# Kernel optimization log

Hardware: AMD Instinct MI355X
Metric: run time of the kernel (lower is better)

The kernel has to match this reference:

```python
import jax, jax.numpy as jnp
import numpy as np

N, R, IN_DIM, OUT_DIM, MODE = 16, 128, 64, 64, 16


def setup_inputs() -> dict:
    key = jax.random.key(0)
    k1, k2, k3, k4, k5 = jax.random.split(key, 5)
    # xavier_normal-like scale used by the torch init:
    # std = gain * sqrt(2/(fan_in+fan_out)) with gain = sqrt(in+out)/(in*out)
    fan = IN_DIM * OUT_DIM * MODE * MODE  # torch fans over last-dim slices; scale is tiny either way
    w_std = (1.0 / (IN_DIM * OUT_DIM)) * np.sqrt(IN_DIM + OUT_DIM)
    return {
        "X": jax.random.normal(k1, (N, R, R, IN_DIM), dtype=jnp.float32),
        "w_res": jax.random.normal(k2, (IN_DIM, OUT_DIM), dtype=jnp.float32) / np.sqrt(IN_DIM),
        "b_res": jax.random.normal(k3, (OUT_DIM,), dtype=jnp.float32) * 0.01,
        "fw0": jax.random.normal(k4, (IN_DIM, OUT_DIM, MODE, MODE, 2), dtype=jnp.float32) * w_std,
        "fw1": jax.random.normal(k5, (IN_DIM, OUT_DIM, MODE, MODE, 2), dtype=jnp.float32) * w_std,
    }


def reference(X, w_res, b_res, fw0, fw1):
    # X: [N, r, r, in_dim]
    n, r, _, _ = X.shape
    m = MODE
    res = X @ w_res + b_res                          # [N, r, r, out]
    Xp = jnp.transpose(X, (0, 3, 1, 2))              # [N, in, r, r]
    X_ft = jnp.fft.rfft2(Xp, s=(r, r), norm="ortho")  # [N, in, r, r//2+1] complex
    W0 = fw0[..., 0] + 1j * fw0[..., 1]              # [in, out, m, m] complex
    W1 = fw1[..., 0] + 1j * fw1[..., 1]
    top = jnp.einsum("nihw,iohw->nohw", X_ft[:, :, :m, :m], W0)
    bot = jnp.einsum("nihw,iohw->nohw", X_ft[:, :, -m:, :m], W1)
    Out_ft = jnp.zeros((n, OUT_DIM, r, r // 2 + 1), dtype=top.dtype)
    Out_ft = Out_ft.at[:, :, :m, :m].set(top)
    Out_ft = Out_ft.at[:, :, -m:, :m].set(bot)
    Y = jnp.fft.irfft2(Out_ft, s=(r, r), norm="ortho")  # [N, out, r, r]
    Y = jnp.transpose(Y, (0, 2, 3, 1))                   # [N, r, r, out]
    return jax.nn.silu(Y + res)
```

## Files before the change

kernel.cpp:

```cpp
#include <hip/hip_runtime.h>

#define NBATCH 16
#define RSZ 128
#define ICH 64
#define OCH 64
#define MODES 16
#define TMODES 32
#define PI2F 6.283185307179586f

typedef float f32x4 __attribute__((ext_vector_type(4)));
typedef short bf16x8 __attribute__((ext_vector_type(8)));

static __device__ __forceinline__ ushort f2bf(float f) {
  union { float f; unsigned u; } v;
  v.f = f;
  unsigned r = v.u + 0x7FFFu + ((v.u >> 16) & 1u);
  return (ushort)(r >> 16);
}
static __device__ __forceinline__ float b2f(ushort u) {
  union { unsigned u; float f; } v;
  v.u = ((unsigned)u) << 16;
  return v.f;
}

#define TAB_EF 4096
#define TAB_WR 8192
#define TAB_T1 12288
#define TAB_E2 28672

__global__ __launch_bounds__(256) void k_main(const float* __restrict__ X,
                                              const float* __restrict__ fw0,
                                              const float* __restrict__ fw1,
                                              const float* __restrict__ w_res,
                                              ushort* __restrict__ Are,
                                              ushort* __restrict__ Aim,
                                              ushort* __restrict__ fwT,
                                              ushort* __restrict__ tabs) {
  const int tid = threadIdx.x;
  if (blockIdx.x >= 512) {
    const int b = blockIdx.x - 512;
    if (b < 128) {
      const int tensor = b >> 6, i = b & 63;
      const float* fw = tensor ? fw1 : fw0;
      const int o = tid & 63, q = tid >> 6;
      const float2* src = (const float2*)fw + ((size_t)(i * 64 + o) * 256 + q * 64);
      ushort2* dst = (ushort2*)fwT;
#pragma unroll 4
      for (int r = 0; r < 64; ++r) {
        float2 v = src[r];
        int mh = q * 4 + (r >> 4), w = r & 15;
        int t = tensor * 16 + mh;
        ushort2 pk;
        pk.x = f2bf(v.x);
        pk.y = f2bf(v.y);
        dst[(((size_t)w * 32 + t) * 64 + i) * 64 + o] = pk;
      }
      return;
    }
    __shared__ float2 ut[128];
    if (tid < 128) {
      float s, c;
      sincosf(PI2F * (float)tid * (1.0f / 128.0f), &s, &c);
      ut[tid] = make_float2(c, s);
    }
    __syncthreads();
    const int pb = b - 128;
    if (pb == 0) {
      for (int e = tid; e < 4096; e += 256) {
        int x = e >> 5, mm = e & 31, w = mm >> 1, c = mm & 1;
        float2 u = ut[(w * x) & 127];
        tabs[TAB_EF + e] = f2bf(c ? -u.y : u.x);
      }
    } else if (pb == 1) {
      for (int e = tid; e < 4096; e += 256) {
        int o = e >> 6, i = e & 63;
        tabs[TAB_WR + e] = f2bf(w_res[i * 64 + o]);
      }
    } else if (pb < 6) {
      for (int k = tid; k < 4096; k += 256) {
        int e = (pb - 2) * 4096 + k;
        int m = e >> 8, kk = e & 255;
        int y = kk & 127, pl = kk >> 7;
        int t = m & 31, imr = m >> 5;
        int h = (t < 16) ? t : (t + 96);
        float2 u = ut[(h * y) & 127];
        float val = (!imr) ? (pl ? u.y : u.x) : (pl ? u.x : -u.y);
        tabs[TAB_T1 + e] = f2bf(val);
      }
    } else {
      for (int k = tid; k < 4096; k += 256) {
        int e = (pb - 6) * 4096 + k;
        int m = e >> 6, kk = e & 63;
        int y = m & 127, imr = m >> 7;
        int t = kk & 31, pl = kk >> 5;
        int h = (t < 16) ? t : (t + 96);
        float2 u = ut[(h * y) & 127];
        float val = (!imr) ? (pl ? -u.y : u.x) : (pl ? u.x : u.y);
        tabs[TAB_E2 + e] = f2bf(val);
      }
    }
    return;
  }
  __shared__ ushort Tm[32][136];
  __shared__ ushort XT[4][64][136];
  const int row0 = blockIdx.x * 4;
  {
    int w = tid >> 4, xseg = (tid & 15) * 8;
    for (int e = 0; e < 8; ++e) {
      int x = xseg + e;
      int p = (w * x) & 127;
      float s, c;
      sincosf(PI2F * (float)p * (1.0f / 128.0f), &s, &c);
      Tm[2 * w][x] = f2bf(c);
      Tm[2 * w + 1][x] = f2bf(-s);
    }
  }
  {
    const int rr = tid >> 6, lane = tid & 63;
    const float* Xr = X + (size_t)(row0 + rr) * RSZ * ICH;
    for (int j = 0; j < 8; ++j) {
      int t = lane + 64 * j;
      int i0 = (t & 15) * 4, x0 = (t >> 4) * 4;
      float4 r0 = *(const float4*)&Xr[(x0 + 0) * ICH + i0];
      float4 r1 = *(const float4*)&Xr[(x0 + 1) * ICH + i0];
      float4 r2 = *(const float4*)&Xr[(x0 + 2) * ICH + i0];
      float4 r3 = *(const float4*)&Xr[(x0 + 3) * ICH + i0];
#pragma unroll
      for (int p = 0; p < 4; ++p) {
        int i = i0 + p;
        int col = x0 ^ ((((i) >> 2) & 7) << 3);
        ushort4 pk;
        pk.x = f2bf(((const float*)&r0)[p]);
        pk.y = f2bf(((const float*)&r1)[p]);
        pk.z = f2bf(((const float*)&r2)[p]);
        pk.w = f2bf(((const float*)&r3)[p]);
        *(ushort4*)&XT[rr][i][col] = pk;
      }
    }
  }
  __syncthreads();
  const int wid = tid >> 6, lane = tid & 63;
  const int lr = lane & 15, lk = lane >> 4;
  f32x4 acc[2][4];
#pragma unroll
  for (int mt = 0; mt < 2; ++mt)
#pragma unroll
    for (int nt = 0; nt < 4; ++nt) acc[mt][nt] = (f32x4)(0.f);
#pragma unroll
  for (int kt = 0; kt < 4; ++kt) {
    int kb = kt * 32 + lk * 8;
    bf16x8 a0 = *(const bf16x8*)&Tm[lr][kb];
    bf16x8 a1 = *(const bf16x8*)&Tm[16 + lr][kb];
    bf16x8 b[4];
#pragma unroll
    for (int nt = 0; nt < 4; ++nt) {
      int i = nt * 16 + lr;
      int col = kb ^ (((i >> 2) & 7) << 3);
      b[nt] = *(const bf16x8*)&XT[wid][i][col];
    }
#pragma unroll
    for (int nt = 0; nt < 4; ++nt) {
      acc[0][nt] = __builtin_amdgcn_mfma_f32_16x16x32_bf16(a0, b[nt], acc[0][nt], 0, 0, 0);
      acc[1][nt] = __builtin_amdgcn_mfma_f32_16x16x32_bf16(a1, b[nt], acc[1][nt], 0, 0, 0);
    }
  }
  const int row = row0 + wid;
#pragma unroll
  for (int mt = 0; mt < 2; ++mt)
#pragma unroll
    for (int q = 0; q < 4; ++q) {
      int m = mt * 16 + lk * 4 + q;
      int w = m >> 1, c = m & 1;
      ushort* plane = c ? Aim : Are;
#pragma unroll
      for (int nt = 0; nt < 4; ++nt) {
        int i = nt * 16 + lr;
        plane[((size_t)row * MODES + w) * ICH + i] = f2bf(acc[mt][nt][q]);
      }
    }
}

__global__ __launch_bounds__(512) void k_mid(const ushort* __restrict__ Are,
                                             const ushort* __restrict__ Aim,
                                             const ushort* __restrict__ tabs,
                                             const ushort* __restrict__ fwT,
                                             ushort* __restrict__ D) {
  const int n = blockIdx.x >> 4;
  const int w = blockIdx.x & 15;
  __shared__ ushort E2s[256][72];
  __shared__ ushort T1s[64][264];
  __shared__ ushort As[64][264];
  __shared__ float2 Bls[32][66];
  __shared__ ushort Cs[64][72];
  const int tid = threadIdx.x;
  {
    int m = tid >> 1, seg = (tid & 1) * 32;
#pragma unroll
    for (int e = 0; e < 4; ++e)
      *(bf16x8*)&E2s[m][seg + e * 8] = *(const bf16x8*)&tabs[TAB_E2 + m * 64 + seg + e * 8];
  }
  {
    int m = tid >> 3, seg = (tid & 7) * 32;
#pragma unroll
    for (int e = 0; e < 4; ++e)
      *(bf16x8*)&T1s[m][seg + e * 8] = *(const bf16x8*)&tabs[TAB_T1 + m * 256 + seg + e * 8];
  }
#pragma unroll
  for (int e = 0; e < 2; ++e) {
    int tt = e * 512 + tid;
    int pl = tt >> 9, r = tt & 511;
    int i0 = (r & 15) * 4, y0 = (r >> 4) * 4;
    const ushort* P = pl ? Aim : Are;
    const ushort* base = P + (((size_t)(n * RSZ + y0) * MODES + w) * ICH + i0);
    ushort4 r0 = *(const ushort4*)(base + 0 * MODES * ICH);
    ushort4 r1 = *(const ushort4*)(base + 1 * MODES * ICH);
    ushort4 r2 = *(const ushort4*)(base + 2 * MODES * ICH);
    ushort4 r3 = *(const ushort4*)(base + 3 * MODES * ICH);
    const ushort* q0 = (const ushort*)&r0;
    const ushort* q1 = (const ushort*)&r1;
    const ushort* q2 = (const ushort*)&r2;
    const ushort* q3 = (const ushort*)&r3;
#pragma unroll
    for (int p = 0; p < 4; ++p) {
      ushort4 pk;
      pk.x = q0[p]; pk.y = q1[p]; pk.z = q2[p]; pk.w = q3[p];
      *(ushort4*)&As[i0 + p][pl * 128 + y0] = pk;
    }
  }
  __syncthreads();
  const int wid = tid >> 6, lane = tid & 63;
  const int lr = lane & 15, lk = lane >> 4;
  {
    const int mt = wid >> 1, nh = wid & 1;
    f32x4 acc[2];
    acc[0] = (f32x4)(0.f);
    acc[1] = (f32x4)(0.f);
#pragma unroll
    for (int kt = 0; kt < 8; ++kt) {
      int kb = kt * 32 + lk * 8;
      bf16x8 a = *(const bf16x8*)&T1s[mt * 16 + lr][kb];
      bf16x8 b0 = *(const bf16x8*)&As[(nh * 2 + 0) * 16 + lr][kb];
      bf16x8 b1 = *(const bf16x8*)&As[(nh * 2 + 1) * 16 + lr][kb];
      acc[0] = __builtin_amdgcn_mfma_f32_16x16x32_bf16(a, b0, acc[0], 0, 0, 0);
      acc[1] = __builtin_amdgcn_mfma_f32_16x16x32_bf16(a, b1, acc[1], 0, 0, 0);
    }
#pragma unroll
    for (int nt2 = 0; nt2 < 2; ++nt2)
#pragma unroll
      for (int q = 0; q < 4; ++q) {
        int m = mt * 16 + lk * 4 + q;
        int t = m & 31, pl = m >> 5;
        int i = (nh * 2 + nt2) * 16 + lr;
        ((float*)&Bls[t][i])[pl] = acc[nt2][q];
      }
  }
  __syncthreads();
  const float sc = (w == 0) ? (1.f / 16384.f) : (2.f / 16384.f);
  float2 cacc[4];
  const ushort2* fwT2 = (const ushort2*)fwT;
#pragma unroll
  for (int p = 0; p < 4; ++p) {
    const int t = p * 8 + wid;
    const ushort2* Wcol = fwT2 + (size_t)(w * 32 + t) * 4096 + lane;
    float cr = 0.f, ci = 0.f;
#pragma unroll 8
    for (int i = 0; i < 64; ++i) {
      ushort2 wv = Wcol[i * 64];
      float wr = b2f(wv.x), wi = b2f(wv.y);
      float2 b = Bls[t][i];
      cr += b.x * wr - b.y * wi;
      ci += b.x * wi + b.y * wr;
    }
    cacc[p] = make_float2(cr * sc, ci * sc);
  }
  __syncthreads();
#pragma unroll
  for (int p = 0; p < 4; ++p) {
    const int t = p * 8 + wid;
    Cs[lane][t] = f2bf(cacc[p].x);
    Cs[lane][t + 32] = f2bf(cacc[p].y);
  }
  __syncthreads();
  f32x4 acc[2][4];
#pragma unroll
  for (int mi = 0; mi < 2; ++mi)
#pragma unroll
    for (int nt = 0; nt < 4; ++nt) acc[mi][nt] = (f32x4)(0.f);
#pragma unroll
  for (int kt = 0; kt < 2; ++kt) {
    int kb = kt * 32 + lk * 8;
    bf16x8 b[4];
#pragma unroll
    for (int nt = 0; nt < 4; ++nt) b[nt] = *(const bf16x8*)&Cs[nt * 16 + lr][kb];
#pragma unroll
    for (int mi = 0; mi < 2; ++mi) {
      bf16x8 a = *(const bf16x8*)&E2s[(wid * 2 + mi) * 16 + lr][kb];
#pragma unroll
      for (int nt = 0; nt < 4; ++nt)
        acc[mi][nt] = __builtin_amdgcn_mfma_f32_16x16x32_bf16(a, b[nt], acc[mi][nt], 0, 0, 0);
    }
  }
#pragma unroll
  for (int mi = 0; mi < 2; ++mi)
#pragma unroll
    for (int nt = 0; nt < 4; ++nt)
#pragma unroll
      for (int q = 0; q < 4; ++q) {
        int m = (wid * 2 + mi) * 16 + lk * 4 + q;
        int y = m & 127, pl = m >> 7;
        int o = nt * 16 + lr;
        D[((size_t)(n * RSZ + y) * MODES + w) * 128 + o * 2 + pl] = f2bf(acc[mi][nt][q]);
      }
}

__global__ __launch_bounds__(256) void k_final(const float* __restrict__ X,
                                               const ushort* __restrict__ D,
                                               const ushort* __restrict__ tabs,
                                               const float* __restrict__ b_res,
                                               float* __restrict__ out) {
  __shared__ ushort Ac[128][104];
  __shared__ ushort Bc[64][104];
  __shared__ float br[64];
  const int tid = threadIdx.x;
  const int row = blockIdx.x;
  const float* Xr = X + (size_t)row * RSZ * ICH;
#pragma unroll
  for (int j = 0; j < 8; ++j) {
    int k = tid + j * 256;
    int x = k >> 4, i0 = (k & 15) * 4;
    float4 v = *(const float4*)&Xr[x * ICH + i0];
    ushort4 pk;
    pk.x = f2bf(v.x); pk.y = f2bf(v.y); pk.z = f2bf(v.z); pk.w = f2bf(v.w);
    *(ushort4*)&Ac[x][i0] = pk;
  }
  {
    int x = tid >> 1, half = tid & 1;
    *(bf16x8*)&Ac[x][64 + half * 16] = *(const bf16x8*)&tabs[TAB_EF + x * 32 + half * 16];
    *(bf16x8*)&Ac[x][64 + half * 16 + 8] = *(const bf16x8*)&tabs[TAB_EF + x * 32 + half * 16 + 8];
  }
  {
    int o = tid >> 2, s = (tid & 3) * 16;
    *(bf16x8*)&Bc[o][s] = *(const bf16x8*)&tabs[TAB_WR + o * 64 + s];
    *(bf16x8*)&Bc[o][s + 8] = *(const bf16x8*)&tabs[TAB_WR + o * 64 + s + 8];
  }
#pragma unroll
  for (int j = 0; j < 4; ++j) {
    int idx = tid + j * 256;
    int w2 = idx >> 6, o = idx & 63;
    ushort2 v = *(const ushort2*)&D[(size_t)row * 2048 + w2 * 128 + o * 2];
    *(ushort2*)&Bc[o][64 + 2 * w2] = v;
  }
  if (tid < 64) br[tid] = b_res[tid];
  __syncthreads();
  const int wid = tid >> 6, lane = tid & 63;
  const int lr = lane & 15, lk = lane >> 4;
  f32x4 acc[2][4];
#pragma unroll
  for (int mi = 0; mi < 2; ++mi)
#pragma unroll
    for (int nt = 0; nt < 4; ++nt) acc[mi][nt] = (f32x4)(0.f);
#pragma unroll
  for (int kt = 0; kt < 3; ++kt) {
    int kb = kt * 32 + lk * 8;
    bf16x8 a0 = *(const bf16x8*)&Ac[(wid * 2 + 0) * 16 + lr][kb];
    bf16x8 a1 = *(const bf16x8*)&Ac[(wid * 2 + 1) * 16 + lr][kb];
    bf16x8 b[4];
#pragma unroll
    for (int nt = 0; nt < 4; ++nt) b[nt] = *(const bf16x8*)&Bc[nt * 16 + lr][kb];
#pragma unroll
    for (int nt = 0; nt < 4; ++nt) {
      acc[0][nt] = __builtin_amdgcn_mfma_f32_16x16x32_bf16(a0, b[nt], acc[0][nt], 0, 0, 0);
      acc[1][nt] = __builtin_amdgcn_mfma_f32_16x16x32_bf16(a1, b[nt], acc[1][nt], 0, 0, 0);
    }
  }
  float* orow = out + (size_t)row * RSZ * OCH;
#pragma unroll
  for (int mi = 0; mi < 2; ++mi)
#pragma unroll
    for (int nt = 0; nt < 4; ++nt)
#pragma unroll
      for (int q = 0; q < 4; ++q) {
        int x = (wid * 2 + mi) * 16 + lk * 4 + q;
        int o = nt * 16 + lr;
        float v = acc[mi][nt][q] + br[o];
        orow[x * OCH + o] = v / (1.f + __expf(-v));
      }
}

extern "C" void kernel_launch(void* const* d_in, const int* in_sizes, int n_in,
                              void* d_out, int out_size, void* d_ws, size_t ws_size,
                              hipStream_t stream) {
  (void)in_sizes; (void)n_in; (void)out_size; (void)ws_size;
  const float* X = (const float*)d_in[0];
  const float* w_res = (const float*)d_in[1];
  const float* b_res = (const float*)d_in[2];
  const float* fw0 = (const float*)d_in[3];
  const float* fw1 = (const float*)d_in[4];
  float* out = (float*)d_out;
  ushort* wsu = (ushort*)d_ws;
  ushort* Are = wsu;
  ushort* Aim = Are + 2097152;
  ushort* Dbf = Aim + 2097152;
  ushort* fwT = Dbf + 4194304;
  ushort* tabs = fwT + 4194304;
  k_main<<<650, 256, 0, stream>>>(X, fw0, fw1, w_res, Are, Aim, fwT, tabs);
  k_mid<<<NBATCH * MODES, 512, 0, stream>>>(Are, Aim, tabs, fwT, Dbf);
  k_final<<<NBATCH * RSZ, 256, 0, stream>>>(X, Dbf, tabs, b_res, out);
}
```

Baseline: 66.75 us.

## Halve rows per DFT block, vectorize weight repack, read twiddle tables from global

The first-stage DFT kernel now processes 2 rows per block instead of 4, with the four waves splitting the channel tiles between them. This doubles the block count to fill more CUs and cuts shared memory per block. The weight-repack path loads float4 instead of float2. The mid kernel no longer stages the T1/E2 twiddle tables into LDS and reads the MFMA A-operands straight from global memory. That lowers LDS use and raises occupancy, but relies on cache hits for repeated global reads.

```diff
diff --git a/kernel.cpp b/kernel.cpp
--- a/kernel.cpp
+++ b/kernel.cpp
@@ -27,6 +27,8 @@
 #define TAB_WR 8192
 #define TAB_T1 12288
 #define TAB_E2 28672
+
+#define DFTX_BLOCKS 1024
 
 __global__ __launch_bounds__(256) void k_main(const float* __restrict__ X,
                                               const float* __restrict__ fw0,
@@ -37,23 +39,26 @@
                                               ushort* __restrict__ fwT,
                                               ushort* __restrict__ tabs) {
   const int tid = threadIdx.x;
-  if (blockIdx.x >= 512) {
-    const int b = blockIdx.x - 512;
+  if (blockIdx.x >= DFTX_BLOCKS) {
+    const int b = blockIdx.x - DFTX_BLOCKS;
     if (b < 128) {
       const int tensor = b >> 6, i = b & 63;
       const float* fw = tensor ? fw1 : fw0;
       const int o = tid & 63, q = tid >> 6;
-      const float2* src = (const float2*)fw + ((size_t)(i * 64 + o) * 256 + q * 64);
+      const float* src = fw + ((size_t)(i * 64 + o) * 256 + q * 64) * 2;
       ushort2* dst = (ushort2*)fwT;
 #pragma unroll 4
-      for (int r = 0; r < 64; ++r) {
-        float2 v = src[r];
-        int mh = q * 4 + (r >> 4), w = r & 15;
-        int t = tensor * 16 + mh;
-        ushort2 pk;
-        pk.x = f2bf(v.x);
-        pk.y = f2bf(v.y);
-        dst[(((size_t)w * 32 + t) * 64 + i) * 64 + o] = pk;
+      for (int r2 = 0; r2 < 32; ++r2) {
+        float4 v = *(const float4*)(src + r2 * 4);
+        int r = r2 * 2;
+        int mh0 = q * 4 + (r >> 4), w0 = r & 15;
+        int mh1 = q * 4 + ((r + 1) >> 4), w1 = (r + 1) & 15;
+        int t0 = tensor * 16 + mh0, t1 = tensor * 16 + mh1;
+        ushort2 p0, p1;
+        p0.x = f2bf(v.x); p0.y = f2bf(v.y);
+        p1.x = f2bf(v.z); p1.y = f2bf(v.w);
+        dst[(((size_t)w0 * 32 + t0) * 64 + i) * 64 + o] = p0;
+        dst[(((size_t)w1 * 32 + t1) * 64 + i) * 64 + o] = p1;
       }
       return;
     }
@@ -102,8 +107,8 @@
     return;
   }
   __shared__ ushort Tm[32][136];
-  __shared__ ushort XT[4][64][136];
-  const int row0 = blockIdx.x * 4;
+  __shared__ ushort XT[2][64][136];
+  const int row0 = blockIdx.x * 2;
   {
     int w = tid >> 4, xseg = (tid & 15) * 8;
     for (int e = 0; e < 8; ++e) {
@@ -115,56 +120,56 @@
       Tm[2 * w + 1][x] = f2bf(-s);
     }
   }
-  {
-    const int rr = tid >> 6, lane = tid & 63;
+#pragma unroll
+  for (int j = 0; j < 4; ++j) {
+    int tt = tid + 256 * j;
+    int rr = tt >> 9, r = tt & 511;
+    int i0 = (r & 15) * 4, x0 = (r >> 4) * 4;
     const float* Xr = X + (size_t)(row0 + rr) * RSZ * ICH;
-    for (int j = 0; j < 8; ++j) {
-      int t = lane + 64 * j;
-      int i0 = (t & 15) * 4, x0 = (t >> 4) * 4;
-      float4 r0 = *(const float4*)&Xr[(x0 + 0) * ICH + i0];
-      float4 r1 = *(const float4*)&Xr[(x0 + 1) * ICH + i0];
-      float4 r2 = *(const float4*)&Xr[(x0 + 2) * ICH + i0];
-      float4 r3 = *(const float4*)&Xr[(x0 + 3) * ICH + i0];
-#pragma unroll
-      for (int p = 0; p < 4; ++p) {
-        int i = i0 + p;
-        int col = x0 ^ ((((i) >> 2) & 7) << 3);
-        ushort4 pk;
-        pk.x = f2bf(((const float*)&r0)[p]);
-        pk.y = f2bf(((const float*)&r1)[p]);
-        pk.z = f2bf(((const float*)&r2)[p]);
-        pk.w = f2bf(((const float*)&r3)[p]);
-        *(ushort4*)&XT[rr][i][col] = pk;
-      }
+    float4 r0 = *(const float4*)&Xr[(x0 + 0) * ICH + i0];
+    float4 r1 = *(const float4*)&Xr[(x0 + 1) * ICH + i0];
+    float4 r2 = *(const float4*)&Xr[(x0 + 2) * ICH + i0];
+    float4 r3 = *(const float4*)&Xr[(x0 + 3) * ICH + i0];
+#pragma unroll
+    for (int p = 0; p < 4; ++p) {
+      int i = i0 + p;
+      int col = x0 ^ ((((i) >> 2) & 7) << 3);
+      ushort4 pk;
+      pk.x = f2bf(((const float*)&r0)[p]);
+      pk.y = f2bf(((const float*)&r1)[p]);
+      pk.z = f2bf(((const float*)&r2)[p]);
+      pk.w = f2bf(((const float*)&r3)[p]);
+      *(ushort4*)&XT[rr][i][col] = pk;
     }
   }
   __syncthreads();
   const int wid = tid >> 6, lane = tid & 63;
   const int lr = lane & 15, lk = lane >> 4;
-  f32x4 acc[2][4];
+  const int rr = wid >> 1, nh = wid & 1;
+  f32x4 acc[2][2];
 #pragma unroll
   for (int mt = 0; mt < 2; ++mt)
 #pragma unroll
-    for (int nt = 0; nt < 4; ++nt) acc[mt][nt] = (f32x4)(0.f);
+    for (int ntl = 0; ntl < 2; ++ntl) acc[mt][ntl] = (f32x4)(0.f);
 #pragma unroll
   for (int kt = 0; kt < 4; ++kt) {
     int kb = kt * 32 + lk * 8;
     bf16x8 a0 = *(const bf16x8*)&Tm[lr][kb];
     bf16x8 a1 = *(const bf16x8*)&Tm[16 + lr][kb];
-    bf16x8 b[4];
-#pragma unroll
-    for (int nt = 0; nt < 4; ++nt) {
-      int i = nt * 16 + lr;
+    bf16x8 b[2];
+#pragma unroll
+    for (int ntl = 0; ntl < 2; ++ntl) {
+      int i = (nh * 2 + ntl) * 16 + lr;
       int col = kb ^ (((i >> 2) & 7) << 3);
-      b[nt] = *(const bf16x8*)&XT[wid][i][col];
-    }
-#pragma unroll
-    for (int nt = 0; nt < 4; ++nt) {
-      acc[0][nt] = __builtin_amdgcn_mfma_f32_16x16x32_bf16(a0, b[nt], acc[0][nt], 0, 0, 0);
-      acc[1][nt] = __builtin_amdgcn_mfma_f32_16x16x32_bf16(a1, b[nt], acc[1][nt], 0, 0, 0);
-    }
-  }
-  const int row = row0 + wid;
+      b[ntl] = *(const bf16x8*)&XT[rr][i][col];
+    }
+#pragma unroll
+    for (int ntl = 0; ntl < 2; ++ntl) {
+      acc[0][ntl] = __builtin_amdgcn_mfma_f32_16x16x32_bf16(a0, b[ntl], acc[0][ntl], 0, 0, 0);
+      acc[1][ntl] = __builtin_amdgcn_mfma_f32_16x16x32_bf16(a1, b[ntl], acc[1][ntl], 0, 0, 0);
+    }
+  }
+  const int row = row0 + rr;
 #pragma unroll
   for (int mt = 0; mt < 2; ++mt)
 #pragma unroll
@@ -173,9 +178,9 @@
       int w = m >> 1, c = m & 1;
       ushort* plane = c ? Aim : Are;
 #pragma unroll
-      for (int nt = 0; nt < 4; ++nt) {
-        int i = nt * 16 + lr;
-        plane[((size_t)row * MODES + w) * ICH + i] = f2bf(acc[mt][nt][q]);
+      for (int ntl = 0; ntl < 2; ++ntl) {
+        int i = (nh * 2 + ntl) * 16 + lr;
+        plane[((size_t)row * MODES + w) * ICH + i] = f2bf(acc[mt][ntl][q]);
       }
     }
 }
@@ -187,24 +192,10 @@
                                              ushort* __restrict__ D) {
   const int n = blockIdx.x >> 4;
   const int w = blockIdx.x & 15;
-  __shared__ ushort E2s[256][72];
-  __shared__ ushort T1s[64][264];
   __shared__ ushort As[64][264];
   __shared__ float2 Bls[32][66];
   __shared__ ushort Cs[64][72];
   const int tid = threadIdx.x;
-  {
-    int m = tid >> 1, seg = (tid & 1) * 32;
-#pragma unroll
-    for (int e = 0; e < 4; ++e)
-      *(bf16x8*)&E2s[m][seg + e * 8] = *(const bf16x8*)&tabs[TAB_E2 + m * 64 + seg + e * 8];
-  }
-  {
-    int m = tid >> 3, seg = (tid & 7) * 32;
-#pragma unroll
-    for (int e = 0; e < 4; ++e)
-      *(bf16x8*)&T1s[m][seg + e * 8] = *(const bf16x8*)&tabs[TAB_T1 + m * 256 + seg + e * 8];
-  }
 #pragma unroll
   for (int e = 0; e < 2; ++e) {
     int tt = e * 512 + tid;
@@ -238,7 +229,7 @@
 #pragma unroll
     for (int kt = 0; kt < 8; ++kt) {
       int kb = kt * 32 + lk * 8;
-      bf16x8 a = *(const bf16x8*)&T1s[mt * 16 + lr][kb];
+      bf16x8 a = *(const bf16x8*)&tabs[TAB_T1 + (mt * 16 + lr) * 256 + kb];
       bf16x8 b0 = *(const bf16x8*)&As[(nh * 2 + 0) * 16 + lr][kb];
       bf16x8 b1 = *(const bf16x8*)&As[(nh * 2 + 1) * 16 + lr][kb];
       acc[0] = __builtin_amdgcn_mfma_f32_16x16x32_bf16(a, b0, acc[0], 0, 0, 0);
@@ -294,7 +285,7 @@
     for (int nt = 0; nt < 4; ++nt) b[nt] = *(const bf16x8*)&Cs[nt * 16 + lr][kb];
 #pragma unroll
     for (int mi = 0; mi < 2; ++mi) {
-      bf16x8 a = *(const bf16x8*)&E2s[(wid * 2 + mi) * 16 + lr][kb];
+      bf16x8 a = *(const bf16x8*)&tabs[TAB_E2 + ((wid * 2 + mi) * 16 + lr) * 64 + kb];
 #pragma unroll
       for (int nt = 0; nt < 4; ++nt)
         acc[mi][nt] = __builtin_amdgcn_mfma_f32_16x16x32_bf16(a, b[nt], acc[mi][nt], 0, 0, 0);
@@ -403,7 +394,7 @@
   ushort* Dbf = Aim + 2097152;
   ushort* fwT = Dbf + 4194304;
   ushort* tabs = fwT + 4194304;
-  k_main<<<650, 256, 0, stream>>>(X, fw0, fw1, w_res, Are, Aim, fwT, tabs);
+  k_main<<<DFTX_BLOCKS + 138, 256, 0, stream>>>(X, fw0, fw1, w_res, Are, Aim, fwT, tabs);
   k_mid<<<NBATCH * MODES, 512, 0, stream>>>(Are, Aim, tabs, fwT, Dbf);
   k_final<<<NBATCH * RSZ, 256, 0, stream>>>(X, Dbf, tabs, b_res, out);
 }
```

Result: slower. 69.08 us (+3.5%).
